# Kernel optimization log

Measured on AMD Instinct MI355X. Metric: run time of the kernel, lower is better.

## Reference

```python
import jax, jax.numpy as jnp
import numpy as np

DIM = 64
CTX = 64
HID = 512
K = 16          # n_bins
TB = 5.0        # tail_bound
N_T = DIM // 2  # n_transform_dims (mask_even=True -> odd indices transformed)
N_P = 3 * K - 1 # params per transformed dim
BATCH = 65536


def setup_inputs() -> dict:
    key = jax.random.key(0)
    ks = jax.random.split(key, 9)
    s = 0.05
    return {
        "x": jax.random.normal(ks[0], (BATCH, DIM), jnp.float32),
        "context": jax.random.normal(ks[1], (BATCH, CTX), jnp.float32),
        "W1": jax.random.normal(ks[2], (DIM + CTX, HID), jnp.float32) * s,
        "b1": jnp.zeros((HID,), jnp.float32),
        "W2": jax.random.normal(ks[3], (HID, HID), jnp.float32) * s,
        "b2": jnp.zeros((HID,), jnp.float32),
        "W3": jax.random.normal(ks[4], (HID, N_T * N_P), jnp.float32) * s,
        "b3": jnp.zeros((N_T * N_P,), jnp.float32),
    }


def _spline_forward(x, raw_params):
    # x: (batch, d); raw_params: (batch, d, 3K-1)
    B = TB
    Wb = jax.nn.softmax(raw_params[..., :K], axis=-1) * (2 * B)       # bin widths
    Hb = jax.nn.softmax(raw_params[..., K:2 * K], axis=-1) * (2 * B)  # bin heights
    D = jax.nn.softplus(raw_params[..., 2 * K:])                      # (batch,d,K-1)
    ones = jnp.ones(D.shape[:-1] + (1,), D.dtype)
    D = jnp.concatenate([ones, D, ones], axis=-1)                     # (batch,d,K+1)

    cumw = jnp.cumsum(Wb, axis=-1) - B
    cumh = jnp.cumsum(Hb, axis=-1) - B
    negB = jnp.full(cumw.shape[:-1] + (1,), -B, cumw.dtype)
    cumw = jnp.concatenate([negB, cumw], axis=-1)                     # (batch,d,K+1)
    cumh = jnp.concatenate([negB, cumh], axis=-1)

    x_c = jnp.clip(x, -B + 1e-06, B - 1e-06)
    # torch.searchsorted left on cumw[...,1:]: count of knots strictly < x
    bin_idx = jnp.sum(cumw[..., 1:] < x_c[..., None], axis=-1)
    bin_idx = jnp.clip(bin_idx, 0, K - 1)[..., None]                  # (batch,d,1)

    take = lambda a: jnp.take_along_axis(a, bin_idx, axis=-1)[..., 0]
    w_k = take(Wb)
    h_k = take(Hb)
    d_k = take(D[..., :-1])
    d_kp1 = take(D[..., 1:])
    cw_k = take(cumw)
    ch_k = take(cumh)

    xi = jnp.clip((x_c - cw_k) / w_k, 0.0, 1.0)
    om = 1.0 - xi
    numerator = h_k * (d_k * xi * xi + 2 * xi * om)
    denominator = d_k + (d_kp1 + d_k - 2) * xi * om
    y = ch_k + numerator / (denominator + 1e-08)
    log_deriv = jnp.log(
        h_k * h_k * (d_kp1 * xi * xi + 2 * xi * om + d_k * om * om)
        / (denominator * denominator * w_k + 1e-08) + 1e-08
    )
    return y, log_deriv


def reference(x, context, W1, b1, W2, b2, W3, b3):
    mask = jnp.zeros((DIM,), x.dtype).at[::2].set(1.0)
    x_masked = x * mask
    inp = jnp.concatenate([x_masked, context], axis=-1)
    h = jax.nn.silu(inp @ W1 + b1)
    h = jax.nn.silu(h @ W2 + b2)
    raw = (h @ W3 + b3).reshape(-1, N_T, N_P)
    x_t = x[:, 1::2]  # mask==0 columns (odd indices)
    y_t, log_det = _spline_forward(x_t, raw)
    y = x.at[:, 1::2].set(y_t)
    return y, jnp.sum(log_det, axis=-1)
```

## Files before the change

### kernel.cpp

```cpp
#include <hip/hip_runtime.h>


typedef _Float16 v8h __attribute__((ext_vector_type(8)));
typedef float v4f __attribute__((ext_vector_type(4)));

#define ROWS_PER_BLOCK 32
#define NBLOCKS (65536 / ROWS_PER_BLOCK)
#define NWAVES 16

#define SMEM_BYTES 150528
#define S_INPLO 8704
#define S_H1HI 17408
#define S_H1LO 50688
#define S_H2HI 83968
#define S_H2LO 117248
#define RAW_STRIDE 388

#define LO_SCALE 2048.f
#define LO_INV   (1.f / 2048.f)

__device__ __forceinline__ void split2(float x, _Float16& hi, _Float16& lo) {
    _Float16 h = (_Float16)x;
    hi = h;
    lo = (_Float16)((x - (float)h) * LO_SCALE);
}
__device__ __forceinline__ float silu_f(float v) {
    return v / (1.f + __expf(-v));
}
__device__ __forceinline__ float softplus_f(float v) {
    return v > 15.f ? v : __logf(1.f + __expf(v));
}

__global__ void nscl_prep_frag(const float* __restrict__ src,
                               _Float16* __restrict__ hi, _Float16* __restrict__ lo,
                               int K, int N) {
    int idx = blockIdx.x * blockDim.x + threadIdx.x;
    if (idx >= N * K) return;
    const int e    = idx & 7;
    const int lane = (idx >> 3) & 63;
    const int rem  = idx >> 9;
    const int KS   = K >> 5;
    const int ks   = rem % KS;
    const int j    = rem / KS;
    const int n = j * 16 + (lane & 15);
    const int k = ks * 32 + ((lane >> 4) << 3) + e;
    split2(src[k * N + n], hi[idx], lo[idx]);
}

template<int KD, int SA, int NPAIRS, bool DOSILU>
__device__ __forceinline__ void gemm_phase(const _Float16* __restrict__ sAhi,
                                           const _Float16* __restrict__ sAlo,
                                           const _Float16* __restrict__ Bhi,
                                           const _Float16* __restrict__ Blo,
                                           const float* __restrict__ bias,
                                           _Float16* __restrict__ sOutHi,
                                           _Float16* __restrict__ sOutLo,
                                           int strideOut, int wave, int lane) {
    constexpr int KS = KD / 32;
    const int lr  = lane & 15;
    const int lkb = (lane >> 4) << 3;
    const int rb  = (lane >> 4) << 2;

    for (int p = wave; p < NPAIRS; p += NWAVES) {
        const int j0 = p * 2;
        v4f m00 = {0,0,0,0}, m10 = {0,0,0,0}, m01 = {0,0,0,0}, m11 = {0,0,0,0};
        v4f c00 = {0,0,0,0}, c10 = {0,0,0,0}, c01 = {0,0,0,0}, c11 = {0,0,0,0};
        #pragma unroll
        for (int ks = 0; ks < KS; ++ks) {
            const int k0 = ks * 32 + lkb;
            v8h a0h = *(const v8h*)(sAhi + lr * SA + k0);
            v8h a0l = *(const v8h*)(sAlo + lr * SA + k0);
            v8h a1h = *(const v8h*)(sAhi + (16 + lr) * SA + k0);
            v8h a1l = *(const v8h*)(sAlo + (16 + lr) * SA + k0);
            const int bo0 = ((j0 * KS + ks) * 64 + lane) * 8;
            const int bo1 = (((j0 + 1) * KS + ks) * 64 + lane) * 8;
            v8h b0h = *(const v8h*)(Bhi + bo0);
            v8h b0l = *(const v8h*)(Blo + bo0);
            v8h b1h = *(const v8h*)(Bhi + bo1);
            v8h b1l = *(const v8h*)(Blo + bo1);
            m00 = __builtin_amdgcn_mfma_f32_16x16x32_f16(a0h, b0h, m00, 0, 0, 0);
            m10 = __builtin_amdgcn_mfma_f32_16x16x32_f16(a1h, b0h, m10, 0, 0, 0);
            m01 = __builtin_amdgcn_mfma_f32_16x16x32_f16(a0h, b1h, m01, 0, 0, 0);
            m11 = __builtin_amdgcn_mfma_f32_16x16x32_f16(a1h, b1h, m11, 0, 0, 0);
            c00 = __builtin_amdgcn_mfma_f32_16x16x32_f16(a0h, b0l, c00, 0, 0, 0);
            c00 = __builtin_amdgcn_mfma_f32_16x16x32_f16(a0l, b0h, c00, 0, 0, 0);
            c10 = __builtin_amdgcn_mfma_f32_16x16x32_f16(a1h, b0l, c10, 0, 0, 0);
            c10 = __builtin_amdgcn_mfma_f32_16x16x32_f16(a1l, b0h, c10, 0, 0, 0);
            c01 = __builtin_amdgcn_mfma_f32_16x16x32_f16(a0h, b1l, c01, 0, 0, 0);
            c01 = __builtin_amdgcn_mfma_f32_16x16x32_f16(a0l, b1h, c01, 0, 0, 0);
            c11 = __builtin_amdgcn_mfma_f32_16x16x32_f16(a1h, b1l, c11, 0, 0, 0);
            c11 = __builtin_amdgcn_mfma_f32_16x16x32_f16(a1l, b1h, c11, 0, 0, 0);
        }
        #pragma unroll
        for (int jj = 0; jj < 2; ++jj) {
            const int col = (j0 + jj) * 16 + lr;
            const float bv = bias[col];
            const v4f mm0 = jj ? m01 : m00;
            const v4f mm1 = jj ? m11 : m10;
            const v4f cc0 = jj ? c01 : c00;
            const v4f cc1 = jj ? c11 : c10;
            #pragma unroll
            for (int r = 0; r < 4; ++r) {
                float v0 = mm0[r] + cc0[r] * LO_INV + bv;
                float v1 = mm1[r] + cc1[r] * LO_INV + bv;
                if (DOSILU) { v0 = silu_f(v0); v1 = silu_f(v1); }
                split2(v0, sOutHi[(rb + r) * strideOut + col],
                           sOutLo[(rb + r) * strideOut + col]);
                split2(v1, sOutHi[(16 + rb + r) * strideOut + col],
                           sOutLo[(16 + rb + r) * strideOut + col]);
            }
        }
    }
}

__device__ __forceinline__ void gemm3_chunk(const _Float16* __restrict__ sH2Hi,
                                            const _Float16* __restrict__ sH2Lo,
                                            const _Float16* __restrict__ W3hi,
                                            const _Float16* __restrict__ W3lo,
                                            const float* __restrict__ b3,
                                            float* __restrict__ sRaw,
                                            int t0, int wave, int lane) {
    const int lr  = lane & 15;
    const int lkb = (lane >> 4) << 3;
    const int rb  = (lane >> 4) << 2;

    for (int tt = wave; tt < 24; tt += NWAVES) {
        const int jt = t0 + tt;
        v4f m0 = {0,0,0,0}, m1 = {0,0,0,0};
        v4f cc0 = {0,0,0,0}, cc1 = {0,0,0,0};
        #pragma unroll
        for (int ks = 0; ks < 16; ++ks) {
            const int k0 = ks * 32 + lkb;
            v8h a0h = *(const v8h*)(sH2Hi + lr * 520 + k0);
            v8h a0l = *(const v8h*)(sH2Lo + lr * 520 + k0);
            v8h a1h = *(const v8h*)(sH2Hi + (16 + lr) * 520 + k0);
            v8h a1l = *(const v8h*)(sH2Lo + (16 + lr) * 520 + k0);
            const int bo = ((jt * 16 + ks) * 64 + lane) * 8;
            v8h bh = *(const v8h*)(W3hi + bo);
            v8h bl = *(const v8h*)(W3lo + bo);
            m0  = __builtin_amdgcn_mfma_f32_16x16x32_f16(a0h, bh, m0, 0, 0, 0);
            m1  = __builtin_amdgcn_mfma_f32_16x16x32_f16(a1h, bh, m1, 0, 0, 0);
            cc0 = __builtin_amdgcn_mfma_f32_16x16x32_f16(a0h, bl, cc0, 0, 0, 0);
            cc0 = __builtin_amdgcn_mfma_f32_16x16x32_f16(a0l, bh, cc0, 0, 0, 0);
            cc1 = __builtin_amdgcn_mfma_f32_16x16x32_f16(a1h, bl, cc1, 0, 0, 0);
            cc1 = __builtin_amdgcn_mfma_f32_16x16x32_f16(a1l, bh, cc1, 0, 0, 0);
        }
        const int col  = jt * 16 + lr;
        const int lcol = tt * 16 + lr;
        const float bv = b3[col];
        #pragma unroll
        for (int r = 0; r < 4; ++r) {
            sRaw[(rb + r) * RAW_STRIDE + lcol]      = m0[r] + cc0[r] * LO_INV + bv;
            sRaw[(16 + rb + r) * RAW_STRIDE + lcol] = m1[r] + cc1[r] * LO_INV + bv;
        }
    }
}

__global__ __launch_bounds__(1024, 4)
void nscl_fused(const float* __restrict__ xp, const float* __restrict__ ctxp,
                const float* __restrict__ b1, const float* __restrict__ b2,
                const float* __restrict__ b3,
                const _Float16* __restrict__ W1Thi, const _Float16* __restrict__ W1Tlo,
                const _Float16* __restrict__ W2Thi, const _Float16* __restrict__ W2Tlo,
                const _Float16* __restrict__ W3Thi, const _Float16* __restrict__ W3Tlo,
                float* __restrict__ outY, float* __restrict__ outLD) {
    __shared__ __align__(16) char smem[SMEM_BYTES];
    _Float16* sInpHi = (_Float16*)smem;
    _Float16* sInpLo = (_Float16*)(smem + S_INPLO);
    _Float16* sH1Hi  = (_Float16*)(smem + S_H1HI);
    _Float16* sH1Lo  = (_Float16*)(smem + S_H1LO);
    _Float16* sH2Hi  = (_Float16*)(smem + S_H2HI);
    _Float16* sH2Lo  = (_Float16*)(smem + S_H2LO);
    float*    sRaw   = (float*)smem;

    const int tid  = threadIdx.x;
    const int lane = tid & 63;
    const int wave = tid >> 6;
    const int row0 = blockIdx.x * ROWS_PER_BLOCK;

    for (int idx = tid; idx < ROWS_PER_BLOCK * 128; idx += 1024) {
        int r = idx >> 7, c = idx & 127;
        float v;
        if (c < 64) v = (c & 1) ? 0.f : xp[(row0 + r) * 64 + c];
        else        v = ctxp[(row0 + r) * 64 + (c - 64)];
        split2(v, sInpHi[r * 136 + c], sInpLo[r * 136 + c]);
    }
    __syncthreads();

    gemm_phase<128, 136, 16, true>(sInpHi, sInpLo, W1Thi, W1Tlo, b1,
                                   sH1Hi, sH1Lo, 520, wave, lane);
    __syncthreads();
    gemm_phase<512, 520, 16, true>(sH1Hi, sH1Lo, W2Thi, W2Tlo, b2,
                                   sH2Hi, sH2Lo, 520, wave, lane);
    __syncthreads();

    const float TB = 5.0f;
    float ldacc = 0.f;
    const int r  = (tid < 256) ? (tid >> 3) : 0;
    const int tl = tid & 7;
    const int t0s[4] = {0, 23, 47, 70};

    #pragma unroll 1
    for (int ch = 0; ch < 4; ++ch) {
        gemm3_chunk(sH2Hi, sH2Lo, W3Thi, W3Tlo, b3, sRaw, t0s[ch], wave, lane);
        __syncthreads();

        if (tid < 256) {
            const int t = ch * 8 + tl;
            const int g = row0 + r;
            const float* pr = sRaw + r * RAW_STRIDE + ((ch & 1) ? 8 : 0) + tl * 47;

            float mw = -1e30f, mh = -1e30f;
            #pragma unroll
            for (int i = 0; i < 16; ++i) {
                mw = fmaxf(mw, pr[i]);
                mh = fmaxf(mh, pr[16 + i]);
            }
            float wv[16], hv[16];
            float sw = 0.f, sh = 0.f;
            #pragma unroll
            for (int i = 0; i < 16; ++i) {
                wv[i] = __expf(pr[i] - mw);       sw += wv[i];
                hv[i] = __expf(pr[16 + i] - mh);  sh += hv[i];
            }
            const float scw = 10.f / sw;
            const float sch = 10.f / sh;

            const float xt = xp[g * 64 + 2 * t + 1];
            const float xc = fminf(fmaxf(xt, -TB + 1e-6f), TB - 1e-6f);

            float cum = -TB; int cnt = 0;
            #pragma unroll
            for (int i = 0; i < 16; ++i) {
                cum += wv[i] * scw;
                cnt += (cum < xc) ? 1 : 0;
            }
            const int bin = cnt > 15 ? 15 : cnt;

            float w_k = 0.f, cw_k = 0.f, h_k = 0.f, ch_k = 0.f;
            float cw = -TB, chh = -TB;
            #pragma unroll
            for (int i = 0; i < 16; ++i) {
                const float wi = wv[i] * scw;
                const float hi = hv[i] * sch;
                if (i == bin) { w_k = wi; cw_k = cw; h_k = hi; ch_k = chh; }
                cw += wi; chh += hi;
            }

            const float d_k  = (bin == 0)  ? 1.f : softplus_f(pr[31 + bin]);
            const float d_k1 = (bin == 15) ? 1.f : softplus_f(pr[32 + bin]);

            float xi = (xc - cw_k) / w_k;
            xi = fminf(fmaxf(xi, 0.f), 1.f);
            const float om = 1.f - xi;
            const float num = h_k * (d_k * xi * xi + 2.f * xi * om);
            const float den = d_k + (d_k1 + d_k - 2.f) * xi * om;
            const float yv  = ch_k + num / (den + 1e-8f);
            const float dv  = h_k * h_k * (d_k1 * xi * xi + 2.f * xi * om + d_k * om * om)
                              / (den * den * w_k + 1e-8f) + 1e-8f;

            float v = __logf(dv);
            v += __shfl_xor(v, 1);
            v += __shfl_xor(v, 2);
            v += __shfl_xor(v, 4);
            ldacc += v;

            outY[g * 64 + 2 * t]     = xp[g * 64 + 2 * t];
            outY[g * 64 + 2 * t + 1] = yv;
        }
        __syncthreads();
    }

    if (tid < 256 && tl == 0) outLD[row0 + r] = ldacc;
}

extern "C" void kernel_launch(void* const* d_in, const int* in_sizes, int n_in,
                              void* d_out, int out_size, void* d_ws, size_t ws_size,
                              hipStream_t stream) {
    (void)in_sizes; (void)n_in; (void)out_size; (void)ws_size;
    const float* x   = (const float*)d_in[0];
    const float* ctx = (const float*)d_in[1];
    const float* W1  = (const float*)d_in[2];
    const float* b1  = (const float*)d_in[3];
    const float* W2  = (const float*)d_in[4];
    const float* b2  = (const float*)d_in[5];
    const float* W3  = (const float*)d_in[6];
    const float* b3  = (const float*)d_in[7];

    _Float16* base = (_Float16*)d_ws;
    _Float16* W1Thi = base;
    _Float16* W1Tlo = base + 65536;
    _Float16* W2Thi = base + 131072;
    _Float16* W2Tlo = base + 393216;
    _Float16* W3Thi = base + 655360;
    _Float16* W3Tlo = base + 1425408;

    nscl_prep_frag<<<(512 * 128 + 255) / 256, 256, 0, stream>>>(W1, W1Thi, W1Tlo, 128, 512);
    nscl_prep_frag<<<(512 * 512 + 255) / 256, 256, 0, stream>>>(W2, W2Thi, W2Tlo, 512, 512);
    nscl_prep_frag<<<(512 * 1504 + 255) / 256, 256, 0, stream>>>(W3, W3Thi, W3Tlo, 512, 1504);

    float* outY  = (float*)d_out;
    float* outLD = outY + 65536 * 64;

    nscl_fused<<<NBLOCKS, 1024, 0, stream>>>(x, ctx, b1, b2, b3,
                                             W1Thi, W1Tlo, W2Thi, W2Tlo, W3Thi, W3Tlo,
                                             outY, outLD);
}
```

Baseline: 713.7 us.

## Store activations in MFMA fragment order and share A fragments across tile pairs

Hidden activations in shared memory now use the MFMA A-fragment layout instead of padded row-major. Each lane's A operand becomes one contiguous 16-byte load, the padding goes away, and the epilogues write straight into fragment order. The third GEMM now gives 12 waves two output tiles each, so A loads are shared across both, where before 16 waves had uneven single-tile work. Input staging is vectorized into packed 8-wide fp16 stores. In exchange the epilogue stores are scattered 2-byte writes, which can cause LDS bank conflicts, and four waves sit idle during the third GEMM.

```diff
diff --git a/kernel.cpp b/kernel.cpp
--- a/kernel.cpp
+++ b/kernel.cpp
@@ -5,15 +5,15 @@
 typedef float v4f __attribute__((ext_vector_type(4)));
 
 #define ROWS_PER_BLOCK 32
-#define NBLOCKS (65536 / ROWS_PER_BLOCK)
+#define NBLOCKS 2048
 #define NWAVES 16
 
-#define SMEM_BYTES 150528
-#define S_INPLO 8704
-#define S_H1HI 17408
-#define S_H1LO 50688
-#define S_H2HI 83968
-#define S_H2LO 117248
+#define SMEM_BYTES 147456
+#define S_INPLO 8192
+#define S_H1HI  16384
+#define S_H1LO  49152
+#define S_H2HI  81920
+#define S_H2LO  114688
 #define RAW_STRIDE 388
 
 #define LO_SCALE 2048.f
@@ -47,111 +47,108 @@
     split2(src[k * N + n], hi[idx], lo[idx]);
 }
 
-template<int KD, int SA, int NPAIRS, bool DOSILU>
-__device__ __forceinline__ void gemm_phase(const _Float16* __restrict__ sAhi,
-                                           const _Float16* __restrict__ sAlo,
-                                           const _Float16* __restrict__ Bhi,
-                                           const _Float16* __restrict__ Blo,
-                                           const float* __restrict__ bias,
-                                           _Float16* __restrict__ sOutHi,
-                                           _Float16* __restrict__ sOutLo,
-                                           int strideOut, int wave, int lane) {
-    constexpr int KS = KD / 32;
-    const int lr  = lane & 15;
-    const int lkb = (lane >> 4) << 3;
-    const int rb  = (lane >> 4) << 2;
-
-    for (int p = wave; p < NPAIRS; p += NWAVES) {
-        const int j0 = p * 2;
-        v4f m00 = {0,0,0,0}, m10 = {0,0,0,0}, m01 = {0,0,0,0}, m11 = {0,0,0,0};
-        v4f c00 = {0,0,0,0}, c10 = {0,0,0,0}, c01 = {0,0,0,0}, c11 = {0,0,0,0};
-        #pragma unroll
-        for (int ks = 0; ks < KS; ++ks) {
-            const int k0 = ks * 32 + lkb;
-            v8h a0h = *(const v8h*)(sAhi + lr * SA + k0);
-            v8h a0l = *(const v8h*)(sAlo + lr * SA + k0);
-            v8h a1h = *(const v8h*)(sAhi + (16 + lr) * SA + k0);
-            v8h a1l = *(const v8h*)(sAlo + (16 + lr) * SA + k0);
-            const int bo0 = ((j0 * KS + ks) * 64 + lane) * 8;
-            const int bo1 = (((j0 + 1) * KS + ks) * 64 + lane) * 8;
-            v8h b0h = *(const v8h*)(Bhi + bo0);
-            v8h b0l = *(const v8h*)(Blo + bo0);
-            v8h b1h = *(const v8h*)(Bhi + bo1);
-            v8h b1l = *(const v8h*)(Blo + bo1);
-            m00 = __builtin_amdgcn_mfma_f32_16x16x32_f16(a0h, b0h, m00, 0, 0, 0);
-            m10 = __builtin_amdgcn_mfma_f32_16x16x32_f16(a1h, b0h, m10, 0, 0, 0);
-            m01 = __builtin_amdgcn_mfma_f32_16x16x32_f16(a0h, b1h, m01, 0, 0, 0);
-            m11 = __builtin_amdgcn_mfma_f32_16x16x32_f16(a1h, b1h, m11, 0, 0, 0);
-            c00 = __builtin_amdgcn_mfma_f32_16x16x32_f16(a0h, b0l, c00, 0, 0, 0);
-            c00 = __builtin_amdgcn_mfma_f32_16x16x32_f16(a0l, b0h, c00, 0, 0, 0);
-            c10 = __builtin_amdgcn_mfma_f32_16x16x32_f16(a1h, b0l, c10, 0, 0, 0);
-            c10 = __builtin_amdgcn_mfma_f32_16x16x32_f16(a1l, b0h, c10, 0, 0, 0);
-            c01 = __builtin_amdgcn_mfma_f32_16x16x32_f16(a0h, b1l, c01, 0, 0, 0);
-            c01 = __builtin_amdgcn_mfma_f32_16x16x32_f16(a0l, b1h, c01, 0, 0, 0);
-            c11 = __builtin_amdgcn_mfma_f32_16x16x32_f16(a1h, b1l, c11, 0, 0, 0);
-            c11 = __builtin_amdgcn_mfma_f32_16x16x32_f16(a1l, b1h, c11, 0, 0, 0);
-        }
-        #pragma unroll
-        for (int jj = 0; jj < 2; ++jj) {
-            const int col = (j0 + jj) * 16 + lr;
-            const float bv = bias[col];
-            const v4f mm0 = jj ? m01 : m00;
-            const v4f mm1 = jj ? m11 : m10;
-            const v4f cc0 = jj ? c01 : c00;
-            const v4f cc1 = jj ? c11 : c10;
-            #pragma unroll
-            for (int r = 0; r < 4; ++r) {
-                float v0 = mm0[r] + cc0[r] * LO_INV + bv;
-                float v1 = mm1[r] + cc1[r] * LO_INV + bv;
-                if (DOSILU) { v0 = silu_f(v0); v1 = silu_f(v1); }
-                split2(v0, sOutHi[(rb + r) * strideOut + col],
-                           sOutLo[(rb + r) * strideOut + col]);
-                split2(v1, sOutHi[(16 + rb + r) * strideOut + col],
-                           sOutLo[(16 + rb + r) * strideOut + col]);
-            }
-        }
-    }
-}
-
-__device__ __forceinline__ void gemm3_chunk(const _Float16* __restrict__ sH2Hi,
-                                            const _Float16* __restrict__ sH2Lo,
-                                            const _Float16* __restrict__ W3hi,
-                                            const _Float16* __restrict__ W3lo,
-                                            const float* __restrict__ b3,
-                                            float* __restrict__ sRaw,
-                                            int t0, int wave, int lane) {
-    const int lr  = lane & 15;
-    const int lkb = (lane >> 4) << 3;
-    const int rb  = (lane >> 4) << 2;
-
-    for (int tt = wave; tt < 24; tt += NWAVES) {
-        const int jt = t0 + tt;
-        v4f m0 = {0,0,0,0}, m1 = {0,0,0,0};
-        v4f cc0 = {0,0,0,0}, cc1 = {0,0,0,0};
-        #pragma unroll
-        for (int ks = 0; ks < 16; ++ks) {
-            const int k0 = ks * 32 + lkb;
-            v8h a0h = *(const v8h*)(sH2Hi + lr * 520 + k0);
-            v8h a0l = *(const v8h*)(sH2Lo + lr * 520 + k0);
-            v8h a1h = *(const v8h*)(sH2Hi + (16 + lr) * 520 + k0);
-            v8h a1l = *(const v8h*)(sH2Lo + (16 + lr) * 520 + k0);
-            const int bo = ((jt * 16 + ks) * 64 + lane) * 8;
-            v8h bh = *(const v8h*)(W3hi + bo);
-            v8h bl = *(const v8h*)(W3lo + bo);
-            m0  = __builtin_amdgcn_mfma_f32_16x16x32_f16(a0h, bh, m0, 0, 0, 0);
-            m1  = __builtin_amdgcn_mfma_f32_16x16x32_f16(a1h, bh, m1, 0, 0, 0);
-            cc0 = __builtin_amdgcn_mfma_f32_16x16x32_f16(a0h, bl, cc0, 0, 0, 0);
-            cc0 = __builtin_amdgcn_mfma_f32_16x16x32_f16(a0l, bh, cc0, 0, 0, 0);
-            cc1 = __builtin_amdgcn_mfma_f32_16x16x32_f16(a1h, bl, cc1, 0, 0, 0);
-            cc1 = __builtin_amdgcn_mfma_f32_16x16x32_f16(a1l, bh, cc1, 0, 0, 0);
-        }
-        const int col  = jt * 16 + lr;
-        const int lcol = tt * 16 + lr;
-        const float bv = b3[col];
-        #pragma unroll
-        for (int r = 0; r < 4; ++r) {
-            sRaw[(rb + r) * RAW_STRIDE + lcol]      = m0[r] + cc0[r] * LO_INV + bv;
-            sRaw[(16 + rb + r) * RAW_STRIDE + lcol] = m1[r] + cc1[r] * LO_INV + bv;
+template<int KS>
+__device__ __forceinline__ void gemm12(const _Float16* __restrict__ sAhi,
+                                       const _Float16* __restrict__ sAlo,
+                                       const _Float16* __restrict__ Bhi,
+                                       const _Float16* __restrict__ Blo,
+                                       const float* __restrict__ bias,
+                                       _Float16* __restrict__ sOutHi,
+                                       _Float16* __restrict__ sOutLo,
+                                       int wave, int lane) {
+    const int j0 = wave * 2;
+    v4f m0[2] = {{0,0,0,0},{0,0,0,0}};
+    v4f m1[2] = {{0,0,0,0},{0,0,0,0}};
+    v4f c0[2] = {{0,0,0,0},{0,0,0,0}};
+    v4f c1[2] = {{0,0,0,0},{0,0,0,0}};
+    #pragma unroll
+    for (int ks = 0; ks < KS; ++ks) {
+        const int abase = (ks * 64 + lane) * 8;
+        v8h a0h = *(const v8h*)(sAhi + abase);
+        v8h a0l = *(const v8h*)(sAlo + abase);
+        v8h a1h = *(const v8h*)(sAhi + KS * 512 + abase);
+        v8h a1l = *(const v8h*)(sAlo + KS * 512 + abase);
+        #pragma unroll
+        for (int i = 0; i < 2; ++i) {
+            const int bo = (((j0 + i) * KS + ks) * 64 + lane) * 8;
+            v8h bh = *(const v8h*)(Bhi + bo);
+            v8h bl = *(const v8h*)(Blo + bo);
+            m0[i] = __builtin_amdgcn_mfma_f32_16x16x32_f16(a0h, bh, m0[i], 0, 0, 0);
+            m1[i] = __builtin_amdgcn_mfma_f32_16x16x32_f16(a1h, bh, m1[i], 0, 0, 0);
+            c0[i] = __builtin_amdgcn_mfma_f32_16x16x32_f16(a0h, bl, c0[i], 0, 0, 0);
+            c0[i] = __builtin_amdgcn_mfma_f32_16x16x32_f16(a0l, bh, c0[i], 0, 0, 0);
+            c1[i] = __builtin_amdgcn_mfma_f32_16x16x32_f16(a1h, bl, c1[i], 0, 0, 0);
+            c1[i] = __builtin_amdgcn_mfma_f32_16x16x32_f16(a1l, bh, c1[i], 0, 0, 0);
+        }
+    }
+    const int r2b = (lane >> 4) * 4;
+    #pragma unroll
+    for (int i = 0; i < 2; ++i) {
+        const int C  = (j0 + i) * 16 + (lane & 15);
+        const int ks2 = C >> 5, g2 = (C >> 3) & 3, e2 = C & 7;
+        const float bv = bias[C];
+        #pragma unroll
+        for (int mt = 0; mt < 2; ++mt) {
+            const v4f mm = mt ? m1[i] : m0[i];
+            const v4f cc = mt ? c1[i] : c0[i];
+            #pragma unroll
+            for (int rr = 0; rr < 4; ++rr) {
+                float v = silu_f(mm[rr] + cc[rr] * LO_INV + bv);
+                const int off = ((mt * 16 + ks2) * 64 + g2 * 16 + r2b + rr) * 8 + e2;
+                split2(v, sOutHi[off], sOutLo[off]);
+            }
+        }
+    }
+}
+
+__device__ __forceinline__ void gemm3(const _Float16* __restrict__ sAhi,
+                                      const _Float16* __restrict__ sAlo,
+                                      const _Float16* __restrict__ Bhi,
+                                      const _Float16* __restrict__ Blo,
+                                      const float* __restrict__ b3,
+                                      float* __restrict__ sRaw,
+                                      int t0, int wave, int lane) {
+    if (wave >= 12) return;
+    const int j0 = t0 + wave * 2;
+    v4f m0[2] = {{0,0,0,0},{0,0,0,0}};
+    v4f m1[2] = {{0,0,0,0},{0,0,0,0}};
+    v4f c0[2] = {{0,0,0,0},{0,0,0,0}};
+    v4f c1[2] = {{0,0,0,0},{0,0,0,0}};
+    #pragma unroll
+    for (int ks = 0; ks < 16; ++ks) {
+        const int abase = (ks * 64 + lane) * 8;
+        v8h a0h = *(const v8h*)(sAhi + abase);
+        v8h a0l = *(const v8h*)(sAlo + abase);
+        v8h a1h = *(const v8h*)(sAhi + 8192 + abase);
+        v8h a1l = *(const v8h*)(sAlo + 8192 + abase);
+        #pragma unroll
+        for (int i = 0; i < 2; ++i) {
+            const int bo = (((j0 + i) * 16 + ks) * 64 + lane) * 8;
+            v8h bh = *(const v8h*)(Bhi + bo);
+            v8h bl = *(const v8h*)(Blo + bo);
+            m0[i] = __builtin_amdgcn_mfma_f32_16x16x32_f16(a0h, bh, m0[i], 0, 0, 0);
+            m1[i] = __builtin_amdgcn_mfma_f32_16x16x32_f16(a1h, bh, m1[i], 0, 0, 0);
+            c0[i] = __builtin_amdgcn_mfma_f32_16x16x32_f16(a0h, bl, c0[i], 0, 0, 0);
+            c0[i] = __builtin_amdgcn_mfma_f32_16x16x32_f16(a0l, bh, c0[i], 0, 0, 0);
+            c1[i] = __builtin_amdgcn_mfma_f32_16x16x32_f16(a1h, bl, c1[i], 0, 0, 0);
+            c1[i] = __builtin_amdgcn_mfma_f32_16x16x32_f16(a1l, bh, c1[i], 0, 0, 0);
+        }
+    }
+    const int r2b = (lane >> 4) * 4;
+    #pragma unroll
+    for (int i = 0; i < 2; ++i) {
+        const int C    = (j0 + i) * 16 + (lane & 15);
+        const int lcol = (j0 + i - t0) * 16 + (lane & 15);
+        const float bv = b3[C];
+        #pragma unroll
+        for (int mt = 0; mt < 2; ++mt) {
+            const v4f mm = mt ? m1[i] : m0[i];
+            const v4f cc = mt ? c1[i] : c0[i];
+            #pragma unroll
+            for (int rr = 0; rr < 4; ++rr) {
+                const int R = mt * 16 + r2b + rr;
+                sRaw[R * RAW_STRIDE + lcol] = mm[rr] + cc[rr] * LO_INV + bv;
+            }
         }
     }
 }
@@ -178,20 +175,39 @@
     const int wave = tid >> 6;
     const int row0 = blockIdx.x * ROWS_PER_BLOCK;
 
-    for (int idx = tid; idx < ROWS_PER_BLOCK * 128; idx += 1024) {
-        int r = idx >> 7, c = idx & 127;
-        float v;
-        if (c < 64) v = (c & 1) ? 0.f : xp[(row0 + r) * 64 + c];
-        else        v = ctxp[(row0 + r) * 64 + (c - 64)];
-        split2(v, sInpHi[r * 136 + c], sInpLo[r * 136 + c]);
+    if (tid < 512) {
+        const int slot = tid;
+        const int mt = slot >> 8;
+        const int ks = (slot >> 6) & 3;
+        const int l  = slot & 63;
+        const int row = mt * 16 + (l & 15);
+        const int c0  = ks * 32 + ((l >> 4) << 3);
+        const int g   = row0 + row;
+        float v[8];
+        if (c0 < 64) {
+            #pragma unroll
+            for (int e = 0; e < 8; ++e)
+                v[e] = ((c0 + e) & 1) ? 0.f : xp[g * 64 + c0 + e];
+        } else {
+            #pragma unroll
+            for (int e = 0; e < 8; ++e)
+                v[e] = ctxp[g * 64 + c0 - 64 + e];
+        }
+        v8h hi8, lo8;
+        #pragma unroll
+        for (int e = 0; e < 8; ++e) {
+            _Float16 h, lo;
+            split2(v[e], h, lo);
+            hi8[e] = h; lo8[e] = lo;
+        }
+        *(v8h*)(sInpHi + slot * 8) = hi8;
+        *(v8h*)(sInpLo + slot * 8) = lo8;
     }
     __syncthreads();
 
-    gemm_phase<128, 136, 16, true>(sInpHi, sInpLo, W1Thi, W1Tlo, b1,
-                                   sH1Hi, sH1Lo, 520, wave, lane);
+    gemm12<4>(sInpHi, sInpLo, W1Thi, W1Tlo, b1, sH1Hi, sH1Lo, wave, lane);
     __syncthreads();
-    gemm_phase<512, 520, 16, true>(sH1Hi, sH1Lo, W2Thi, W2Tlo, b2,
-                                   sH2Hi, sH2Lo, 520, wave, lane);
+    gemm12<16>(sH1Hi, sH1Lo, W2Thi, W2Tlo, b2, sH2Hi, sH2Lo, wave, lane);
     __syncthreads();
 
     const float TB = 5.0f;
@@ -202,7 +218,7 @@
 
     #pragma unroll 1
     for (int ch = 0; ch < 4; ++ch) {
-        gemm3_chunk(sH2Hi, sH2Lo, W3Thi, W3Tlo, b3, sRaw, t0s[ch], wave, lane);
+        gemm3(sH2Hi, sH2Lo, W3Thi, W3Tlo, b3, sRaw, t0s[ch], wave, lane);
         __syncthreads();
 
         if (tid < 256) {
```

Result: slower. 920.4 us (+29.0%).

## Store activations in MFMA fragment order and recompute softmax exps to cut registers

Applied to the files above, without the earlier changes.

The input and hidden activation tiles in shared memory are now written directly in the MFMA A-fragment order. Each lane then loads its operand as one contiguous 16-byte read instead of a strided row access, and the padded row strides go away, so shared memory shrinks slightly. The GEMM loop for layers 1 and 2 is specialised so each wave owns exactly one column pair. In the spline stage, the 32-element exp arrays are dropped and the exps are recomputed in each pass, trading extra transcendental work for lower register pressure.

```diff
diff --git a/kernel.cpp b/kernel.cpp
--- a/kernel.cpp
+++ b/kernel.cpp
@@ -5,15 +5,15 @@
 typedef float v4f __attribute__((ext_vector_type(4)));
 
 #define ROWS_PER_BLOCK 32
-#define NBLOCKS (65536 / ROWS_PER_BLOCK)
+#define NBLOCKS 2048
 #define NWAVES 16
 
-#define SMEM_BYTES 150528
-#define S_INPLO 8704
-#define S_H1HI 17408
-#define S_H1LO 50688
-#define S_H2HI 83968
-#define S_H2LO 117248
+#define SMEM_BYTES 147456
+#define S_INPLO 8192
+#define S_H1HI  16384
+#define S_H1LO  49152
+#define S_H2HI  81920
+#define S_H2LO  114688
 #define RAW_STRIDE 388
 
 #define LO_SCALE 2048.f
@@ -47,97 +47,87 @@
     split2(src[k * N + n], hi[idx], lo[idx]);
 }
 
-template<int KD, int SA, int NPAIRS, bool DOSILU>
-__device__ __forceinline__ void gemm_phase(const _Float16* __restrict__ sAhi,
-                                           const _Float16* __restrict__ sAlo,
-                                           const _Float16* __restrict__ Bhi,
-                                           const _Float16* __restrict__ Blo,
-                                           const float* __restrict__ bias,
-                                           _Float16* __restrict__ sOutHi,
-                                           _Float16* __restrict__ sOutLo,
-                                           int strideOut, int wave, int lane) {
-    constexpr int KS = KD / 32;
-    const int lr  = lane & 15;
-    const int lkb = (lane >> 4) << 3;
-    const int rb  = (lane >> 4) << 2;
-
-    for (int p = wave; p < NPAIRS; p += NWAVES) {
-        const int j0 = p * 2;
-        v4f m00 = {0,0,0,0}, m10 = {0,0,0,0}, m01 = {0,0,0,0}, m11 = {0,0,0,0};
-        v4f c00 = {0,0,0,0}, c10 = {0,0,0,0}, c01 = {0,0,0,0}, c11 = {0,0,0,0};
+template<int KS>
+__device__ __forceinline__ void gemm12(const _Float16* __restrict__ sAhi,
+                                       const _Float16* __restrict__ sAlo,
+                                       const _Float16* __restrict__ Bhi,
+                                       const _Float16* __restrict__ Blo,
+                                       const float* __restrict__ bias,
+                                       _Float16* __restrict__ sOutHi,
+                                       _Float16* __restrict__ sOutLo,
+                                       int wave, int lane) {
+    const int j0 = wave * 2;
+    v4f m00 = {0,0,0,0}, m10 = {0,0,0,0}, m01 = {0,0,0,0}, m11 = {0,0,0,0};
+    v4f c00 = {0,0,0,0}, c10 = {0,0,0,0}, c01 = {0,0,0,0}, c11 = {0,0,0,0};
+    #pragma unroll
+    for (int ks = 0; ks < KS; ++ks) {
+        const int ab = (ks * 64 + lane) * 8;
+        v8h a0h = *(const v8h*)(sAhi + ab);
+        v8h a0l = *(const v8h*)(sAlo + ab);
+        v8h a1h = *(const v8h*)(sAhi + KS * 512 + ab);
+        v8h a1l = *(const v8h*)(sAlo + KS * 512 + ab);
+        const int bo0 = ((j0 * KS + ks) * 64 + lane) * 8;
+        const int bo1 = (((j0 + 1) * KS + ks) * 64 + lane) * 8;
+        v8h b0h = *(const v8h*)(Bhi + bo0);
+        v8h b0l = *(const v8h*)(Blo + bo0);
+        v8h b1h = *(const v8h*)(Bhi + bo1);
+        v8h b1l = *(const v8h*)(Blo + bo1);
+        m00 = __builtin_amdgcn_mfma_f32_16x16x32_f16(a0h, b0h, m00, 0, 0, 0);
+        m10 = __builtin_amdgcn_mfma_f32_16x16x32_f16(a1h, b0h, m10, 0, 0, 0);
+        m01 = __builtin_amdgcn_mfma_f32_16x16x32_f16(a0h, b1h, m01, 0, 0, 0);
+        m11 = __builtin_amdgcn_mfma_f32_16x16x32_f16(a1h, b1h, m11, 0, 0, 0);
+        c00 = __builtin_amdgcn_mfma_f32_16x16x32_f16(a0h, b0l, c00, 0, 0, 0);
+        c00 = __builtin_amdgcn_mfma_f32_16x16x32_f16(a0l, b0h, c00, 0, 0, 0);
+        c10 = __builtin_amdgcn_mfma_f32_16x16x32_f16(a1h, b0l, c10, 0, 0, 0);
+        c10 = __builtin_amdgcn_mfma_f32_16x16x32_f16(a1l, b0h, c10, 0, 0, 0);
+        c01 = __builtin_amdgcn_mfma_f32_16x16x32_f16(a0h, b1l, c01, 0, 0, 0);
+        c01 = __builtin_amdgcn_mfma_f32_16x16x32_f16(a0l, b1h, c01, 0, 0, 0);
+        c11 = __builtin_amdgcn_mfma_f32_16x16x32_f16(a1h, b1l, c11, 0, 0, 0);
+        c11 = __builtin_amdgcn_mfma_f32_16x16x32_f16(a1l, b1h, c11, 0, 0, 0);
+    }
+    const int r2b = (lane >> 4) * 4;
+    #pragma unroll
+    for (int jj = 0; jj < 2; ++jj) {
+        const int C   = (j0 + jj) * 16 + (lane & 15);
+        const int ks2 = C >> 5, g2 = (C >> 3) & 3, e2 = C & 7;
+        const float bv = bias[C];
+        const v4f mm0 = jj ? m01 : m00;
+        const v4f mm1 = jj ? m11 : m10;
+        const v4f cc0 = jj ? c01 : c00;
+        const v4f cc1 = jj ? c11 : c10;
         #pragma unroll
-        for (int ks = 0; ks < KS; ++ks) {
-            const int k0 = ks * 32 + lkb;
-            v8h a0h = *(const v8h*)(sAhi + lr * SA + k0);
-            v8h a0l = *(const v8h*)(sAlo + lr * SA + k0);
-            v8h a1h = *(const v8h*)(sAhi + (16 + lr) * SA + k0);
-            v8h a1l = *(const v8h*)(sAlo + (16 + lr) * SA + k0);
-            const int bo0 = ((j0 * KS + ks) * 64 + lane) * 8;
-            const int bo1 = (((j0 + 1) * KS + ks) * 64 + lane) * 8;
-            v8h b0h = *(const v8h*)(Bhi + bo0);
-            v8h b0l = *(const v8h*)(Blo + bo0);
-            v8h b1h = *(const v8h*)(Bhi + bo1);
-            v8h b1l = *(const v8h*)(Blo + bo1);
-            m00 = __builtin_amdgcn_mfma_f32_16x16x32_f16(a0h, b0h, m00, 0, 0, 0);
-            m10 = __builtin_amdgcn_mfma_f32_16x16x32_f16(a1h, b0h, m10, 0, 0, 0);
-            m01 = __builtin_amdgcn_mfma_f32_16x16x32_f16(a0h, b1h, m01, 0, 0, 0);
-            m11 = __builtin_amdgcn_mfma_f32_16x16x32_f16(a1h, b1h, m11, 0, 0, 0);
-            c00 = __builtin_amdgcn_mfma_f32_16x16x32_f16(a0h, b0l, c00, 0, 0, 0);
-            c00 = __builtin_amdgcn_mfma_f32_16x16x32_f16(a0l, b0h, c00, 0, 0, 0);
-            c10 = __builtin_amdgcn_mfma_f32_16x16x32_f16(a1h, b0l, c10, 0, 0, 0);
-            c10 = __builtin_amdgcn_mfma_f32_16x16x32_f16(a1l, b0h, c10, 0, 0, 0);
-            c01 = __builtin_amdgcn_mfma_f32_16x16x32_f16(a0h, b1l, c01, 0, 0, 0);
-            c01 = __builtin_amdgcn_mfma_f32_16x16x32_f16(a0l, b1h, c01, 0, 0, 0);
-            c11 = __builtin_amdgcn_mfma_f32_16x16x32_f16(a1h, b1l, c11, 0, 0, 0);
-            c11 = __builtin_amdgcn_mfma_f32_16x16x32_f16(a1l, b1h, c11, 0, 0, 0);
-        }
-        #pragma unroll
-        for (int jj = 0; jj < 2; ++jj) {
-            const int col = (j0 + jj) * 16 + lr;
-            const float bv = bias[col];
-            const v4f mm0 = jj ? m01 : m00;
-            const v4f mm1 = jj ? m11 : m10;
-            const v4f cc0 = jj ? c01 : c00;
-            const v4f cc1 = jj ? c11 : c10;
-            #pragma unroll
-            for (int r = 0; r < 4; ++r) {
-                float v0 = mm0[r] + cc0[r] * LO_INV + bv;
-                float v1 = mm1[r] + cc1[r] * LO_INV + bv;
-                if (DOSILU) { v0 = silu_f(v0); v1 = silu_f(v1); }
-                split2(v0, sOutHi[(rb + r) * strideOut + col],
-                           sOutLo[(rb + r) * strideOut + col]);
-                split2(v1, sOutHi[(16 + rb + r) * strideOut + col],
-                           sOutLo[(16 + rb + r) * strideOut + col]);
-            }
-        }
-    }
-}
-
-__device__ __forceinline__ void gemm3_chunk(const _Float16* __restrict__ sH2Hi,
-                                            const _Float16* __restrict__ sH2Lo,
-                                            const _Float16* __restrict__ W3hi,
-                                            const _Float16* __restrict__ W3lo,
-                                            const float* __restrict__ b3,
-                                            float* __restrict__ sRaw,
-                                            int t0, int wave, int lane) {
-    const int lr  = lane & 15;
-    const int lkb = (lane >> 4) << 3;
-    const int rb  = (lane >> 4) << 2;
-
+        for (int rr = 0; rr < 4; ++rr) {
+            float v0 = silu_f(mm0[rr] + cc0[rr] * LO_INV + bv);
+            float v1 = silu_f(mm1[rr] + cc1[rr] * LO_INV + bv);
+            const int off0 = ((0 * 16 + ks2) * 64 + g2 * 16 + r2b + rr) * 8 + e2;
+            const int off1 = ((1 * 16 + ks2) * 64 + g2 * 16 + r2b + rr) * 8 + e2;
+            split2(v0, sOutHi[off0], sOutLo[off0]);
+            split2(v1, sOutHi[off1], sOutLo[off1]);
+        }
+    }
+}
+
+__device__ __forceinline__ void gemm3(const _Float16* __restrict__ sAhi,
+                                      const _Float16* __restrict__ sAlo,
+                                      const _Float16* __restrict__ Bhi,
+                                      const _Float16* __restrict__ Blo,
+                                      const float* __restrict__ b3,
+                                      float* __restrict__ sRaw,
+                                      int t0, int wave, int lane) {
     for (int tt = wave; tt < 24; tt += NWAVES) {
         const int jt = t0 + tt;
         v4f m0 = {0,0,0,0}, m1 = {0,0,0,0};
         v4f cc0 = {0,0,0,0}, cc1 = {0,0,0,0};
         #pragma unroll
         for (int ks = 0; ks < 16; ++ks) {
-            const int k0 = ks * 32 + lkb;
-            v8h a0h = *(const v8h*)(sH2Hi + lr * 520 + k0);
-            v8h a0l = *(const v8h*)(sH2Lo + lr * 520 + k0);
-            v8h a1h = *(const v8h*)(sH2Hi + (16 + lr) * 520 + k0);
-            v8h a1l = *(const v8h*)(sH2Lo + (16 + lr) * 520 + k0);
+            const int ab = (ks * 64 + lane) * 8;
+            v8h a0h = *(const v8h*)(sAhi + ab);
+            v8h a0l = *(const v8h*)(sAlo + ab);
+            v8h a1h = *(const v8h*)(sAhi + 8192 + ab);
+            v8h a1l = *(const v8h*)(sAlo + 8192 + ab);
             const int bo = ((jt * 16 + ks) * 64 + lane) * 8;
-            v8h bh = *(const v8h*)(W3hi + bo);
-            v8h bl = *(const v8h*)(W3lo + bo);
+            v8h bh = *(const v8h*)(Bhi + bo);
+            v8h bl = *(const v8h*)(Blo + bo);
             m0  = __builtin_amdgcn_mfma_f32_16x16x32_f16(a0h, bh, m0, 0, 0, 0);
             m1  = __builtin_amdgcn_mfma_f32_16x16x32_f16(a1h, bh, m1, 0, 0, 0);
             cc0 = __builtin_amdgcn_mfma_f32_16x16x32_f16(a0h, bl, cc0, 0, 0, 0);
@@ -145,13 +135,14 @@
             cc1 = __builtin_amdgcn_mfma_f32_16x16x32_f16(a1h, bl, cc1, 0, 0, 0);
             cc1 = __builtin_amdgcn_mfma_f32_16x16x32_f16(a1l, bh, cc1, 0, 0, 0);
         }
-        const int col  = jt * 16 + lr;
+        const int lr   = lane & 15;
         const int lcol = tt * 16 + lr;
-        const float bv = b3[col];
+        const float bv = b3[jt * 16 + lr];
+        const int r2b  = (lane >> 4) * 4;
         #pragma unroll
-        for (int r = 0; r < 4; ++r) {
-            sRaw[(rb + r) * RAW_STRIDE + lcol]      = m0[r] + cc0[r] * LO_INV + bv;
-            sRaw[(16 + rb + r) * RAW_STRIDE + lcol] = m1[r] + cc1[r] * LO_INV + bv;
+        for (int rr = 0; rr < 4; ++rr) {
+            sRaw[(r2b + rr) * RAW_STRIDE + lcol]      = m0[rr] + cc0[rr] * LO_INV + bv;
+            sRaw[(16 + r2b + rr) * RAW_STRIDE + lcol] = m1[rr] + cc1[rr] * LO_INV + bv;
         }
     }
 }
@@ -178,31 +169,41 @@
     const int wave = tid >> 6;
     const int row0 = blockIdx.x * ROWS_PER_BLOCK;
 
-    for (int idx = tid; idx < ROWS_PER_BLOCK * 128; idx += 1024) {
-        int r = idx >> 7, c = idx & 127;
-        float v;
-        if (c < 64) v = (c & 1) ? 0.f : xp[(row0 + r) * 64 + c];
-        else        v = ctxp[(row0 + r) * 64 + (c - 64)];
-        split2(v, sInpHi[r * 136 + c], sInpLo[r * 136 + c]);
+    if (tid < 512) {
+        const int mt = tid >> 8;
+        const int l  = tid & 63;
+        const int row = mt * 16 + (l & 15);
+        const int c0  = ((tid >> 6) & 3) * 32 + ((l >> 4) << 3);
+        const int g   = row0 + row;
+        v8h hi8, lo8;
+        #pragma unroll
+        for (int e = 0; e < 8; ++e) {
+            float v;
+            if (c0 < 64) v = ((c0 + e) & 1) ? 0.f : xp[g * 64 + c0 + e];
+            else         v = ctxp[g * 64 + c0 - 64 + e];
+            _Float16 h = (_Float16)v;
+            hi8[e] = h;
+            lo8[e] = (_Float16)((v - (float)h) * LO_SCALE);
+        }
+        *(v8h*)(sInpHi + tid * 8) = hi8;
+        *(v8h*)(sInpLo + tid * 8) = lo8;
     }
     __syncthreads();
 
-    gemm_phase<128, 136, 16, true>(sInpHi, sInpLo, W1Thi, W1Tlo, b1,
-                                   sH1Hi, sH1Lo, 520, wave, lane);
+    gemm12<4>(sInpHi, sInpLo, W1Thi, W1Tlo, b1, sH1Hi, sH1Lo, wave, lane);
     __syncthreads();
-    gemm_phase<512, 520, 16, true>(sH1Hi, sH1Lo, W2Thi, W2Tlo, b2,
-                                   sH2Hi, sH2Lo, 520, wave, lane);
+    gemm12<16>(sH1Hi, sH1Lo, W2Thi, W2Tlo, b2, sH2Hi, sH2Lo, wave, lane);
     __syncthreads();
 
     const float TB = 5.0f;
     float ldacc = 0.f;
     const int r  = (tid < 256) ? (tid >> 3) : 0;
     const int tl = tid & 7;
-    const int t0s[4] = {0, 23, 47, 70};
 
     #pragma unroll 1
     for (int ch = 0; ch < 4; ++ch) {
-        gemm3_chunk(sH2Hi, sH2Lo, W3Thi, W3Tlo, b3, sRaw, t0s[ch], wave, lane);
+        const int t0 = (ch * 47) >> 1;
+        gemm3(sH2Hi, sH2Lo, W3Thi, W3Tlo, b3, sRaw, t0, wave, lane);
         __syncthreads();
 
         if (tid < 256) {
@@ -216,12 +217,11 @@
                 mw = fmaxf(mw, pr[i]);
                 mh = fmaxf(mh, pr[16 + i]);
             }
-            float wv[16], hv[16];
             float sw = 0.f, sh = 0.f;
             #pragma unroll
             for (int i = 0; i < 16; ++i) {
-                wv[i] = __expf(pr[i] - mw);       sw += wv[i];
-                hv[i] = __expf(pr[16 + i] - mh);  sh += hv[i];
+                sw += __expf(pr[i] - mw);
+                sh += __expf(pr[16 + i] - mh);
             }
             const float scw = 10.f / sw;
             const float sch = 10.f / sh;
@@ -232,7 +232,7 @@
             float cum = -TB; int cnt = 0;
             #pragma unroll
             for (int i = 0; i < 16; ++i) {
-                cum += wv[i] * scw;
+                cum += __expf(pr[i] - mw) * scw;
                 cnt += (cum < xc) ? 1 : 0;
             }
             const int bin = cnt > 15 ? 15 : cnt;
@@ -241,8 +241,8 @@
             float cw = -TB, chh = -TB;
             #pragma unroll
             for (int i = 0; i < 16; ++i) {
-                const float wi = wv[i] * scw;
-                const float hi = hv[i] * sch;
+                const float wi = __expf(pr[i] - mw) * scw;
+                const float hi = __expf(pr[16 + i] - mh) * sch;
                 if (i == bin) { w_k = wi; cw_k = cw; h_k = hi; ch_k = chh; }
                 cw += wi; chh += hi;
             }
```

Result: slower. 1.104 ms (+54.7%).
